# Kernel optimization log

Hardware: AMD Instinct MI355X
Metric: run time of the kernel (lower is better)

The kernel has to match this reference:

```python
import jax, jax.numpy as jnp
import numpy as np

DIM = 1280
HEADS = 16
HEAD_DIM = DIM // HEADS  # 80
N_CHUNKS = 8
CHUNK = 1024
TOTAL = N_CHUNKS * CHUNK  # 8192 packed tokens


def rotate_half(x):
    x1, x2 = jnp.split(x, 2, axis=-1)
    return jnp.concatenate([-x2, x1], axis=-1)


def setup_inputs() -> dict:
    key = jax.random.key(0)
    k0, k1, k2 = jax.random.split(key, 3)
    hidden_states = jax.random.normal(k0, (TOTAL, DIM), dtype=jnp.float32)
    # 2D-rope style per-token angles, duplicated halves (standard vision RoPE layout)
    inv_freq = 1.0 / (10000.0 ** (jnp.arange(0, HEAD_DIM, 2, dtype=jnp.float32) / HEAD_DIM))
    pos = jnp.arange(TOTAL, dtype=jnp.float32)
    freqs = pos[:, None] * inv_freq[None, :]            # [T, HEAD_DIM//2]
    emb = jnp.concatenate([freqs, freqs], axis=-1)      # [T, HEAD_DIM]
    cos = jnp.cos(emb)
    sin = jnp.sin(emb)
    qkv_w = jax.random.normal(k1, (3 * DIM, DIM), dtype=jnp.float32) * 0.02
    qkv_b = jnp.zeros((3 * DIM,), dtype=jnp.float32)
    proj_w = jax.random.normal(k2, (DIM, DIM), dtype=jnp.float32) * 0.02
    proj_b = jnp.zeros((DIM,), dtype=jnp.float32)
    cu_seqlens = (jnp.arange(N_CHUNKS + 1, dtype=jnp.int32) * CHUNK)
    return {"hidden_states": hidden_states, "cos": cos, "sin": sin,
            "qkv_w": qkv_w, "qkv_b": qkv_b, "proj_w": proj_w, "proj_b": proj_b,
            "cu_seqlens": cu_seqlens}


def reference(hidden_states, cos, sin, qkv_w, qkv_b, proj_w, proj_b, cu_seqlens):
    # Equal-length chunks (cu_seqlens uniform): vectorize the Python chunk loop
    # as a leading batch axis n over chunks of length L.
    n = cu_seqlens.shape[0] - 1
    total, dim = hidden_states.shape
    L = total // n
    scaling = HEAD_DIM ** -0.5

    x = hidden_states.reshape(n, L, dim)
    qkv = x @ qkv_w.T + qkv_b                              # [n, L, 3*dim]
    qkv = qkv.reshape(n, L, 3, HEADS, HEAD_DIM)
    q, k, v = qkv[:, :, 0], qkv[:, :, 1], qkv[:, :, 2]     # [n, L, H, hd]

    # inline RoPE in fp32 (matches apply_rotary_pos_emb_vision)
    c = cos.reshape(n, L, 1, HEAD_DIM).astype(jnp.float32)
    s = sin.reshape(n, L, 1, HEAD_DIM).astype(jnp.float32)
    qf = q.astype(jnp.float32)
    kf = k.astype(jnp.float32)
    q = (qf * c + rotate_half(qf) * s).astype(q.dtype)
    k = (kf * c + rotate_half(kf) * s).astype(k.dtype)

    # naive per-chunk full attention: QK^T, fp32 softmax, PV
    scores = jnp.einsum('nlhd,nmhd->nhlm', q, k) * scaling  # [n, H, L, L]
    probs = jax.nn.softmax(scores.astype(jnp.float32), axis=-1).astype(q.dtype)
    out = jnp.einsum('nhlm,nmhd->nlhd', probs, v)           # [n, L, H, hd]
    out = out.reshape(n, L, dim)
    out = out @ proj_w.T + proj_b                           # [n, L, dim]
    return out.reshape(total, dim)
```

## Files before the change

### kernel.cpp

```cpp
#include <hip/hip_runtime.h>
#include <stdint.h>

#define DIM 1280
#define HEADS 16
#define HD 80
#define TOTAL 8192
#define CHUNK 1024
#define QKVN 3840

typedef __attribute__((ext_vector_type(8))) __bf16 bf16x8;
typedef __attribute__((ext_vector_type(4))) float floatx4;

typedef __attribute__((address_space(1))) const uint32_t gu32;
typedef __attribute__((address_space(3))) uint32_t lu32;

__device__ __forceinline__ void llds16(const void* g, void* l) {
  __builtin_amdgcn_global_load_lds((gu32*)g, (lu32*)l, 16, 0, 0);
}

__device__ __forceinline__ unsigned short f2b(float f) {
  union { __bf16 b; unsigned short u; } x; x.b = (__bf16)f; return x.u;
}
__device__ __forceinline__ float b2f(unsigned short u) {
  union { __bf16 b; unsigned short u; } x; x.u = u; return (float)x.b;
}
__device__ __forceinline__ float fexp2(float x) {
#if __has_builtin(__builtin_amdgcn_exp2f)
  return __builtin_amdgcn_exp2f(x);
#else
  return __expf(x * 0.6931471805599453f);
#endif
}

#define QSCALE (0.11180339887498949f * 1.44269504088896340f)

#define QROW 96
#define KT_SH (64 * 104)
#define VT_SH (80 * 72)

__global__ void cvt_bf16(const float* __restrict__ src, unsigned short* __restrict__ dst, int n4) {
  int i = blockIdx.x * 256 + threadIdx.x;
  if (i >= n4) return;
  float4 v = reinterpret_cast<const float4*>(src)[i];
  ushort4 o;
  o.x = f2b(v.x); o.y = f2b(v.y); o.z = f2b(v.z); o.w = f2b(v.w);
  reinterpret_cast<ushort4*>(dst)[i] = o;
}

template<int MODE>
__launch_bounds__(256, 2)
__global__ void gemm_bt(const unsigned short* __restrict__ A,
                        const unsigned short* __restrict__ B,
                        const float* __restrict__ bias,
                        unsigned short* __restrict__ qo,
                        unsigned short* __restrict__ ko,
                        unsigned short* __restrict__ vo,
                        float* __restrict__ fo) {
  __shared__ __attribute__((aligned(16))) unsigned short lsA[128 * 32];
  __shared__ __attribute__((aligned(16))) unsigned short lsB[128 * 32];
  const int m0 = blockIdx.x * 128;
  const int n0 = blockIdx.y * 128;
  const int tid = threadIdx.x;
  const int wv = tid >> 6, lane = tid & 63;
  const int wr = wv >> 1, wc = wv & 1;
  const int q4 = lane >> 4, l15 = lane & 15;

  floatx4 acc[4][4];
#pragma unroll
  for (int i = 0; i < 4; ++i)
#pragma unroll
    for (int j = 0; j < 4; ++j)
      acc[i][j] = (floatx4){0.f, 0.f, 0.f, 0.f};

  const int srow = lane >> 2;
  const int sslot = lane & 3;

  for (int kk = 0; kk < DIM; kk += 32) {
    __syncthreads();
#pragma unroll
    for (int t = 0; t < 2; ++t) {
      const int rbase = wv * 32 + t * 16;
      const int r = rbase + srow;
      const int sg = sslot ^ ((r >> 1) & 3);
      llds16(A + (size_t)(m0 + r) * DIM + kk + sg * 8, &lsA[rbase * 32]);
      llds16(B + (size_t)(n0 + r) * DIM + kk + sg * 8, &lsB[rbase * 32]);
    }
    __syncthreads();
    bf16x8 af[4], bfr[4];
#pragma unroll
    for (int i = 0; i < 4; ++i) {
      const int r = wr * 64 + i * 16 + l15;
      af[i] = *reinterpret_cast<const bf16x8*>(&lsA[r * 32 + ((q4 ^ ((r >> 1) & 3)) << 3)]);
      const int c = wc * 64 + i * 16 + l15;
      bfr[i] = *reinterpret_cast<const bf16x8*>(&lsB[c * 32 + ((q4 ^ ((c >> 1) & 3)) << 3)]);
    }
#pragma unroll
    for (int i = 0; i < 4; ++i)
#pragma unroll
      for (int j = 0; j < 4; ++j)
        acc[i][j] = __builtin_amdgcn_mfma_f32_16x16x32_bf16(af[i], bfr[j], acc[i][j], 0, 0, 0);
  }

#pragma unroll
  for (int i = 0; i < 4; ++i) {
#pragma unroll
    for (int j = 0; j < 4; ++j) {
      const int n = n0 + wc * 64 + j * 16 + l15;
      const float bn = bias[n];
#pragma unroll
      for (int r = 0; r < 4; ++r) {
        const int m = m0 + wr * 64 + i * 16 + q4 * 4 + r;
        const float val = acc[i][j][r] + bn;
        if (MODE == 0) {
          if (n < DIM)            qo[(size_t)m * DIM + n] = f2b(val);
          else if (n < 2 * DIM)   ko[(size_t)m * DIM + (n - DIM)] = f2b(val);
          else                    vo[(size_t)m * DIM + (n - 2 * DIM)] = f2b(val);
        } else {
          fo[(size_t)m * DIM + n] = val;
        }
      }
    }
  }
}

__global__ void prep_q(const unsigned short* __restrict__ qbuf,
                       const float* __restrict__ cp, const float* __restrict__ sp,
                       unsigned short* __restrict__ qimg) {
  const int m = blockIdx.x, tid = threadIdx.x;
  const int ch = m >> 10, rl = m & 1023;
#pragma unroll
  for (int i = 0; i < 3; ++i) {
    const int it = i * 256 + tid;
    if (it < 640) {
      const int h = it / 40, d = it - h * 40;
      const float c = cp[m * HD + d], s = sp[m * HD + d];
      const float x1 = b2f(qbuf[(size_t)m * DIM + h * HD + d]);
      const float x2 = b2f(qbuf[(size_t)m * DIM + h * HD + d + 40]);
      const size_t ob = ((size_t)(ch * 16 + h) * 1024 + rl) * QROW;
      qimg[ob + d]      = f2b((x1 * c - x2 * s) * QSCALE);
      qimg[ob + d + 40] = f2b((x2 * c + x1 * s) * QSCALE);
    }
  }
  { const int h = tid >> 4, c = tid & 15;
    qimg[((size_t)(ch * 16 + h) * 1024 + rl) * QROW + 80 + c] = 0; }
}

__global__ void prep_k(const unsigned short* __restrict__ kbuf,
                       const float* __restrict__ cp, const float* __restrict__ sp,
                       unsigned short* __restrict__ kimg) {
  const int m = blockIdx.x, tid = threadIdx.x;
  const int ch = m >> 10, rl = m & 1023;
  const int jt = rl >> 6, rr = rl & 63;
#pragma unroll
  for (int i = 0; i < 3; ++i) {
    const int it = i * 256 + tid;
    if (it < 640) {
      const int h = it / 40, d = it - h * 40;
      const float c = cp[m * HD + d], s = sp[m * HD + d];
      const float x1 = b2f(kbuf[(size_t)m * DIM + h * HD + d]);
      const float x2 = b2f(kbuf[(size_t)m * DIM + h * HD + d + 40]);
      const size_t ob = ((size_t)((ch * 16 + h) * 16 + jt) * KT_SH) + rr * 104;
      kimg[ob + d]      = f2b(x1 * c - x2 * s);
      kimg[ob + d + 40] = f2b(x2 * c + x1 * s);
    }
  }
#pragma unroll
  for (int i = 0; i < 2; ++i) {
    const int it = i * 256 + tid;
    if (it < 384) {
      const int h = it / 24, c = it - h * 24;
      kimg[((size_t)((ch * 16 + h) * 16 + jt) * KT_SH) + rr * 104 + 80 + c] = 0;
    }
  }
}

__global__ void prep_v(const unsigned short* __restrict__ vbuf,
                       unsigned short* __restrict__ vimg) {
  __shared__ __attribute__((aligned(16))) unsigned short lsT[64 * 88];
  const int bx = blockIdx.x;
  const int jt = bx & 15, h = (bx >> 4) & 15, ch = bx >> 8;
  const int tid = threadIdx.x;
  const int row0 = ch * CHUNK + jt * 64;
#pragma unroll
  for (int i = 0; i < 3; ++i) {
    const int it = i * 256 + tid;
    if (it < 640) {
      const int r = it / 10, c = it - r * 10;
      const uint4 v = *reinterpret_cast<const uint4*>(vbuf + (size_t)(row0 + r) * DIM + h * HD + c * 8);
      *reinterpret_cast<uint4*>(&lsT[r * 88 + c * 8]) = v;
    }
  }
  __syncthreads();
  unsigned short* ot = vimg + (size_t)((ch * 16 + h) * 16 + jt) * VT_SH;
#pragma unroll
  for (int i = 0; i < 12; ++i) {
    const int it = i * 256 + tid;
    if (it < 2880) {
      const int d = it / 36, kk = it - d * 36;
      uint32_t w = 0;
      if (kk < 32) {
        const uint32_t lo = lsT[(2 * kk) * 88 + d];
        const uint32_t hi = lsT[(2 * kk + 1) * 88 + d];
        w = lo | (hi << 16);
      }
      *reinterpret_cast<uint32_t*>(ot + d * 72 + kk * 2) = w;
    }
  }
}

__launch_bounds__(256, 3)
__global__ void attn_k(const unsigned short* __restrict__ qimg,
                       const unsigned short* __restrict__ kimg,
                       const unsigned short* __restrict__ vimg,
                       unsigned short* __restrict__ ob) {
  __shared__ __attribute__((aligned(16))) unsigned short lsK[KT_SH];
  __shared__ __attribute__((aligned(16))) unsigned short lsV[VT_SH];
  __shared__ __attribute__((aligned(16))) unsigned short lsP[128 * 72];

  const int bx = blockIdx.x;
  const int qt = bx & 7, h = (bx >> 3) & 15, ch = bx >> 7;
  const int tid = threadIdx.x, wv = tid >> 6, lane = tid & 63;
  const int q4 = lane >> 4, l15 = lane & 15;
  const int qrow_loc = qt * 128 + wv * 32;

  bf16x8 aq[2][3];
  {
    const unsigned short* qb = qimg + ((size_t)(ch * 16 + h) * 1024 + qrow_loc) * QROW;
#pragma unroll
    for (int mt = 0; mt < 2; ++mt)
#pragma unroll
      for (int ks = 0; ks < 3; ++ks)
        aq[mt][ks] = *reinterpret_cast<const bf16x8*>(qb + (size_t)(mt * 16 + l15) * QROW + ks * 32 + q4 * 8);
  }

  floatx4 oacc[2][5];
  float lpart[2] = {0.f, 0.f};
#pragma unroll
  for (int mt = 0; mt < 2; ++mt)
#pragma unroll
    for (int t = 0; t < 5; ++t) oacc[mt][t] = (floatx4){0.f, 0.f, 0.f, 0.f};

  const char* kbase = (const char*)(kimg + (size_t)(ch * 16 + h) * 16 * KT_SH);
  const char* vbase = (const char*)(vimg + (size_t)(ch * 16 + h) * 16 * VT_SH);

  for (int jt = 0; jt < 16; ++jt) {
    __syncthreads();
    {
      const char* kg = kbase + (size_t)jt * (KT_SH * 2);
#pragma unroll
      for (int r = 0; r < 4; ++r) {
        const int off = (r * 4 + wv) * 1024;
        if (off < KT_SH * 2)
          llds16(kg + off + lane * 16, (char*)lsK + off);
      }
      const char* vg = vbase + (size_t)jt * (VT_SH * 2);
#pragma unroll
      for (int r = 0; r < 3; ++r) {
        const int off = (r * 4 + wv) * 1024;
        if (off < VT_SH * 2) {
          if (off + 1024 <= VT_SH * 2) llds16(vg + off + lane * 16, (char*)lsV + off);
          else if (lane < 16)          llds16(vg + off + lane * 16, (char*)lsV + off);
        }
      }
    }
    __syncthreads();

    floatx4 sfr[2][4];
#pragma unroll
    for (int c = 0; c < 4; ++c) {
      const bf16x8 ak0 = *reinterpret_cast<const bf16x8*>(&lsK[(c * 16 + l15) * 104 + 0  + q4 * 8]);
      const bf16x8 ak1 = *reinterpret_cast<const bf16x8*>(&lsK[(c * 16 + l15) * 104 + 32 + q4 * 8]);
      const bf16x8 ak2 = *reinterpret_cast<const bf16x8*>(&lsK[(c * 16 + l15) * 104 + 64 + q4 * 8]);
#pragma unroll
      for (int mt = 0; mt < 2; ++mt) {
        floatx4 s = (floatx4){0.f, 0.f, 0.f, 0.f};
        s = __builtin_amdgcn_mfma_f32_16x16x32_bf16(ak0, aq[mt][0], s, 0, 0, 0);
        s = __builtin_amdgcn_mfma_f32_16x16x32_bf16(ak1, aq[mt][1], s, 0, 0, 0);
        s = __builtin_amdgcn_mfma_f32_16x16x32_bf16(ak2, aq[mt][2], s, 0, 0, 0);
        sfr[mt][c] = s;
      }
    }

#pragma unroll
    for (int mt = 0; mt < 2; ++mt)
#pragma unroll
      for (int c = 0; c < 4; ++c) {
        const float p0 = fexp2(sfr[mt][c][0]);
        const float p1 = fexp2(sfr[mt][c][1]);
        const float p2 = fexp2(sfr[mt][c][2]);
        const float p3 = fexp2(sfr[mt][c][3]);
        lpart[mt] += (p0 + p1) + (p2 + p3);
        ushort4 w;
        w.x = f2b(p0); w.y = f2b(p1); w.z = f2b(p2); w.w = f2b(p3);
        *reinterpret_cast<ushort4*>(&lsP[(wv * 32 + mt * 16 + l15) * 72 + c * 16 + q4 * 4]) = w;
      }

#pragma unroll
    for (int ks = 0; ks < 2; ++ks) {
      const bf16x8 ap0 = *reinterpret_cast<const bf16x8*>(&lsP[(wv * 32 + 0  + l15) * 72 + ks * 32 + q4 * 8]);
      const bf16x8 ap1 = *reinterpret_cast<const bf16x8*>(&lsP[(wv * 32 + 16 + l15) * 72 + ks * 32 + q4 * 8]);
#pragma unroll
      for (int t = 0; t < 5; ++t) {
        const bf16x8 bv = *reinterpret_cast<const bf16x8*>(&lsV[(t * 16 + l15) * 72 + ks * 32 + q4 * 8]);
        oacc[0][t] = __builtin_amdgcn_mfma_f32_16x16x32_bf16(ap0, bv, oacc[0][t], 0, 0, 0);
        oacc[1][t] = __builtin_amdgcn_mfma_f32_16x16x32_bf16(ap1, bv, oacc[1][t], 0, 0, 0);
      }
    }
  }

#pragma unroll
  for (int mt = 0; mt < 2; ++mt) {
    lpart[mt] += __shfl_xor(lpart[mt], 16, 64);
    lpart[mt] += __shfl_xor(lpart[mt], 32, 64);
  }
  float inv[2];
  inv[0] = 1.0f / lpart[0];
  inv[1] = 1.0f / lpart[1];

  float invr[2][4];
#pragma unroll
  for (int mt = 0; mt < 2; ++mt)
#pragma unroll
    for (int r = 0; r < 4; ++r)
      invr[mt][r] = __shfl(inv[mt], q4 * 4 + r, 64);

#pragma unroll
  for (int mt = 0; mt < 2; ++mt)
#pragma unroll
    for (int t = 0; t < 5; ++t)
#pragma unroll
      for (int r = 0; r < 4; ++r) {
        const int gr = ch * CHUNK + qrow_loc + mt * 16 + q4 * 4 + r;
        const int gc = h * HD + t * 16 + l15;
        ob[(size_t)gr * DIM + gc] = f2b(oacc[mt][t][r] * invr[mt][r]);
      }
}

extern "C" void kernel_launch(void* const* d_in, const int* in_sizes, int n_in,
                              void* d_out, int out_size, void* d_ws, size_t ws_size,
                              hipStream_t stream) {
  (void)in_sizes; (void)n_in; (void)out_size; (void)ws_size;
  const float* hs    = (const float*)d_in[0];
  const float* cosp  = (const float*)d_in[1];
  const float* sinp  = (const float*)d_in[2];
  const float* qkvw  = (const float*)d_in[3];
  const float* qkvb  = (const float*)d_in[4];
  const float* projw = (const float*)d_in[5];
  const float* projb = (const float*)d_in[6];

  char* ws = (char*)d_ws;
  unsigned short* xb   = (unsigned short*)(ws + 0);
  unsigned short* wq   = (unsigned short*)(ws + 20971520);
  unsigned short* qbuf = (unsigned short*)(ws + 30801920);
  unsigned short* kbuf = (unsigned short*)(ws + 51773440);
  unsigned short* vbuf = (unsigned short*)(ws + 72744960);
  unsigned short* wp   = (unsigned short*)(ws + 93716480);
  unsigned short* obuf = (unsigned short*)(ws + 96993280);
  unsigned short* kimg = (unsigned short*)(ws + 117964800);
  unsigned short* qimg = (unsigned short*)(ws + 0);
  unsigned short* vimg = (unsigned short*)(ws + 30801920);

  cvt_bf16<<<TOTAL * DIM / 4 / 256, 256, 0, stream>>>(hs, xb, TOTAL * DIM / 4);
  cvt_bf16<<<QKVN * DIM / 4 / 256, 256, 0, stream>>>(qkvw, wq, QKVN * DIM / 4);
  cvt_bf16<<<DIM * DIM / 4 / 256, 256, 0, stream>>>(projw, wp, DIM * DIM / 4);

  gemm_bt<0><<<dim3(TOTAL / 128, QKVN / 128), 256, 0, stream>>>(
      xb, wq, qkvb, qbuf, kbuf, vbuf, nullptr);

  prep_q<<<TOTAL, 256, 0, stream>>>(qbuf, cosp, sinp, qimg);
  prep_k<<<TOTAL, 256, 0, stream>>>(kbuf, cosp, sinp, kimg);
  prep_v<<<2048, 256, 0, stream>>>(vbuf, vimg);

  attn_k<<<1024, 256, 0, stream>>>(qimg, kimg, vimg, obuf);

  gemm_bt<1><<<dim3(TOTAL / 128, DIM / 128), 256, 0, stream>>>(
      obuf, wp, projb, nullptr, nullptr, nullptr, (float*)d_out);
}
```

Measured before the change: 383.4 us.

## Replace GEMM with 256x256 tile, 8-wave, double-buffered ping-pong pipeline

Rewrites both projection GEMMs to use 256x256 output tiles with 512 threads, a K-step of 64 and double-buffered LDS. Global-to-LDS loads for the next K-tile are split into four phases interleaved with MFMA blocks, using manual vmcnt waits, barriers and s_setprio. This aims to hide memory latency and raise arithmetic intensity over the single-buffered 128x128 kernel. The trade-offs are 128KB of LDS per block, which limits occupancy, and fewer blocks for the output projection GEMM (32x5 = 160 tiles), which may underfill the CUs.

```diff
diff --git a/kernel.cpp b/kernel.cpp
--- a/kernel.cpp
+++ b/kernel.cpp
@@ -47,77 +47,193 @@
   reinterpret_cast<ushort4*>(dst)[i] = o;
 }
 
+
+__device__ __forceinline__ void stage_a64(const unsigned short* __restrict__ G,
+                                          unsigned short* ls, int wv, int lane,
+                                          int row0, int kk, int hi) {
+#pragma unroll
+  for (int t = 0; t < 2; ++t) {
+    const int stripe = t * 8 + wv;
+    const int rb = ((stripe >> 3) << 7) + ((stripe & 7) << 3) + hi;
+    const int r = rb + (lane >> 3);
+    const int ch = (lane & 7) ^ (r & 7);
+    llds16(G + (size_t)(row0 + r) * DIM + kk + (ch << 3), ls + rb * 64);
+  }
+}
+
+__device__ __forceinline__ void stage_b64(const unsigned short* __restrict__ G,
+                                          unsigned short* ls, int wv, int lane,
+                                          int row0, int kk, int hi) {
+#pragma unroll
+  for (int t = 0; t < 2; ++t) {
+    const int stripe = t * 8 + wv;
+    const int rb = ((stripe >> 2) << 6) + ((stripe & 3) << 3) + hi;
+    const int r = rb + (lane >> 3);
+    const int ch = (lane & 7) ^ (r & 7);
+    llds16(G + (size_t)(row0 + r) * DIM + kk + (ch << 3), ls + rb * 64);
+  }
+}
+
+__device__ __forceinline__ bf16x8 frg(const unsigned short* ls, int r, int cx) {
+  return *reinterpret_cast<const bf16x8*>(ls + r * 64 + (cx << 3));
+}
+
+#define PH_PRE()                                          \
+  __builtin_amdgcn_s_barrier();                           \
+  asm volatile("s_waitcnt lgkmcnt(0)" ::: "memory");      \
+  __builtin_amdgcn_sched_barrier(0);                      \
+  __builtin_amdgcn_s_setprio(1)
+
+#define PH_POST() __builtin_amdgcn_s_setprio(0)
+
 template<int MODE>
-__launch_bounds__(256, 2)
-__global__ void gemm_bt(const unsigned short* __restrict__ A,
-                        const unsigned short* __restrict__ B,
-                        const float* __restrict__ bias,
-                        unsigned short* __restrict__ qo,
-                        unsigned short* __restrict__ ko,
-                        unsigned short* __restrict__ vo,
-                        float* __restrict__ fo) {
-  __shared__ __attribute__((aligned(16))) unsigned short lsA[128 * 32];
-  __shared__ __attribute__((aligned(16))) unsigned short lsB[128 * 32];
-  const int m0 = blockIdx.x * 128;
-  const int n0 = blockIdx.y * 128;
+__launch_bounds__(512, 2)
+__global__ void gemm8(const unsigned short* __restrict__ A,
+                      const unsigned short* __restrict__ B,
+                      const float* __restrict__ bias,
+                      unsigned short* __restrict__ qo,
+                      unsigned short* __restrict__ ko,
+                      unsigned short* __restrict__ vo,
+                      float* __restrict__ fo) {
+  __shared__ __attribute__((aligned(16))) unsigned short lsA[2][256 * 64];
+  __shared__ __attribute__((aligned(16))) unsigned short lsB[2][256 * 64];
+  const int m0 = blockIdx.x * 256;
+  const int n0 = blockIdx.y * 256;
   const int tid = threadIdx.x;
   const int wv = tid >> 6, lane = tid & 63;
-  const int wr = wv >> 1, wc = wv & 1;
+  const int wr = wv >> 2, wc = wv & 3;
   const int q4 = lane >> 4, l15 = lane & 15;
-
-  floatx4 acc[4][4];
-#pragma unroll
-  for (int i = 0; i < 4; ++i)
+  const int sx = l15 & 7;
+  const int cx0 = q4 ^ sx;
+  const int cx1 = (4 + q4) ^ sx;
+
+  stage_a64(A, &lsA[0][0], wv, lane, m0, 0, 0);
+  stage_b64(B, &lsB[0][0], wv, lane, n0, 0, 0);
+  stage_b64(B, &lsB[0][0], wv, lane, n0, 0, 32);
+  stage_a64(A, &lsA[0][0], wv, lane, m0, 0, 64);
+
+  floatx4 acc[8][4];
+#pragma unroll
+  for (int i = 0; i < 8; ++i)
 #pragma unroll
     for (int j = 0; j < 4; ++j)
       acc[i][j] = (floatx4){0.f, 0.f, 0.f, 0.f};
 
-  const int srow = lane >> 2;
-  const int sslot = lane & 3;
-
-  for (int kk = 0; kk < DIM; kk += 32) {
-    __syncthreads();
-#pragma unroll
-    for (int t = 0; t < 2; ++t) {
-      const int rbase = wv * 32 + t * 16;
-      const int r = rbase + srow;
-      const int sg = sslot ^ ((r >> 1) & 3);
-      llds16(A + (size_t)(m0 + r) * DIM + kk + sg * 8, &lsA[rbase * 32]);
-      llds16(B + (size_t)(n0 + r) * DIM + kk + sg * 8, &lsB[rbase * 32]);
-    }
-    __syncthreads();
-    bf16x8 af[4], bfr[4];
-#pragma unroll
-    for (int i = 0; i < 4; ++i) {
-      const int r = wr * 64 + i * 16 + l15;
-      af[i] = *reinterpret_cast<const bf16x8*>(&lsA[r * 32 + ((q4 ^ ((r >> 1) & 3)) << 3)]);
-      const int c = wc * 64 + i * 16 + l15;
-      bfr[i] = *reinterpret_cast<const bf16x8*>(&lsB[c * 32 + ((q4 ^ ((c >> 1) & 3)) << 3)]);
-    }
-#pragma unroll
-    for (int i = 0; i < 4; ++i)
-#pragma unroll
-      for (int j = 0; j < 4; ++j)
-        acc[i][j] = __builtin_amdgcn_mfma_f32_16x16x32_bf16(af[i], bfr[j], acc[i][j], 0, 0, 0);
-  }
-
-#pragma unroll
-  for (int i = 0; i < 4; ++i) {
-#pragma unroll
-    for (int j = 0; j < 4; ++j) {
-      const int n = n0 + wc * 64 + j * 16 + l15;
-      const float bn = bias[n];
+  asm volatile("s_waitcnt vmcnt(4)" ::: "memory");
+  __builtin_amdgcn_s_barrier();
+
+  const int rA = wr * 128 + l15;
+  const int rB = wc * 64 + l15;
+
+#pragma unroll 2
+  for (int kt = 0; kt < 20; ++kt) {
+    const unsigned short* la = &lsA[kt & 1][0];
+    const unsigned short* lb = &lsB[kt & 1][0];
+    unsigned short* sa = &lsA[(kt & 1) ^ 1][0];
+    unsigned short* sb = &lsB[(kt & 1) ^ 1][0];
+    const int kn = (kt + 1) * 64;
+    const bool st = (kt < 19);
+
+    bf16x8 Ar[4][2], Br[2][2];
+
+#pragma unroll
+    for (int m = 0; m < 4; ++m) {
+      Ar[m][0] = frg(la, rA + m * 16, cx0);
+      Ar[m][1] = frg(la, rA + m * 16, cx1);
+    }
+#pragma unroll
+    for (int n = 0; n < 2; ++n) {
+      Br[n][0] = frg(lb, rB + n * 16, cx0);
+      Br[n][1] = frg(lb, rB + n * 16, cx1);
+    }
+    if (st) stage_a64(A, sa, wv, lane, m0, kn, 0);
+    PH_PRE();
+#pragma unroll
+    for (int m = 0; m < 4; ++m)
+#pragma unroll
+      for (int n = 0; n < 2; ++n) {
+        acc[m][n] = __builtin_amdgcn_mfma_f32_16x16x32_bf16(Ar[m][0], Br[n][0], acc[m][n], 0, 0, 0);
+        acc[m][n] = __builtin_amdgcn_mfma_f32_16x16x32_bf16(Ar[m][1], Br[n][1], acc[m][n], 0, 0, 0);
+      }
+    PH_POST();
+    if (st) asm volatile("s_waitcnt vmcnt(4)" ::: "memory");
+    else    asm volatile("s_waitcnt vmcnt(2)" ::: "memory");
+    __builtin_amdgcn_s_barrier();
+
+#pragma unroll
+    for (int n = 0; n < 2; ++n) {
+      Br[n][0] = frg(lb, rB + (n + 2) * 16, cx0);
+      Br[n][1] = frg(lb, rB + (n + 2) * 16, cx1);
+    }
+    if (st) stage_b64(B, sb, wv, lane, n0, kn, 0);
+    PH_PRE();
+#pragma unroll
+    for (int m = 0; m < 4; ++m)
+#pragma unroll
+      for (int n = 0; n < 2; ++n) {
+        acc[m][n + 2] = __builtin_amdgcn_mfma_f32_16x16x32_bf16(Ar[m][0], Br[n][0], acc[m][n + 2], 0, 0, 0);
+        acc[m][n + 2] = __builtin_amdgcn_mfma_f32_16x16x32_bf16(Ar[m][1], Br[n][1], acc[m][n + 2], 0, 0, 0);
+      }
+    PH_POST();
+    if (st) asm volatile("s_waitcnt vmcnt(4)" ::: "memory");
+    else    asm volatile("s_waitcnt vmcnt(0)" ::: "memory");
+    __builtin_amdgcn_s_barrier();
+
+#pragma unroll
+    for (int m = 0; m < 4; ++m) {
+      Ar[m][0] = frg(la, rA + (m + 4) * 16, cx0);
+      Ar[m][1] = frg(la, rA + (m + 4) * 16, cx1);
+    }
+    if (st) stage_b64(B, sb, wv, lane, n0, kn, 32);
+    PH_PRE();
+#pragma unroll
+    for (int m = 0; m < 4; ++m)
+#pragma unroll
+      for (int n = 0; n < 2; ++n) {
+        acc[m + 4][n + 2] = __builtin_amdgcn_mfma_f32_16x16x32_bf16(Ar[m][0], Br[n][0], acc[m + 4][n + 2], 0, 0, 0);
+        acc[m + 4][n + 2] = __builtin_amdgcn_mfma_f32_16x16x32_bf16(Ar[m][1], Br[n][1], acc[m + 4][n + 2], 0, 0, 0);
+      }
+    PH_POST();
+    __builtin_amdgcn_s_barrier();
+
+#pragma unroll
+    for (int n = 0; n < 2; ++n) {
+      Br[n][0] = frg(lb, rB + n * 16, cx0);
+      Br[n][1] = frg(lb, rB + n * 16, cx1);
+    }
+    if (st) stage_a64(A, sa, wv, lane, m0, kn, 64);
+    PH_PRE();
+#pragma unroll
+    for (int m = 0; m < 4; ++m)
+#pragma unroll
+      for (int n = 0; n < 2; ++n) {
+        acc[m + 4][n] = __builtin_amdgcn_mfma_f32_16x16x32_bf16(Ar[m][0], Br[n][0], acc[m + 4][n], 0, 0, 0);
+        acc[m + 4][n] = __builtin_amdgcn_mfma_f32_16x16x32_bf16(Ar[m][1], Br[n][1], acc[m + 4][n], 0, 0, 0);
+      }
+    PH_POST();
+    if (st) asm volatile("s_waitcnt vmcnt(4)" ::: "memory");
+    __builtin_amdgcn_s_barrier();
+  }
+
+  unsigned short* os = nullptr;
+  int nloc = n0;
+  if (MODE == 0) {
+    if (blockIdx.y < 5)       { os = qo; }
+    else if (blockIdx.y < 10) { os = ko; nloc = n0 - DIM; }
+    else                      { os = vo; nloc = n0 - 2 * DIM; }
+  }
+#pragma unroll
+  for (int n = 0; n < 4; ++n) {
+    const int cg = wc * 64 + n * 16 + l15;
+    const float bn = bias[n0 + cg];
+#pragma unroll
+    for (int m = 0; m < 8; ++m) {
 #pragma unroll
       for (int r = 0; r < 4; ++r) {
-        const int m = m0 + wr * 64 + i * 16 + q4 * 4 + r;
-        const float val = acc[i][j][r] + bn;
-        if (MODE == 0) {
-          if (n < DIM)            qo[(size_t)m * DIM + n] = f2b(val);
-          else if (n < 2 * DIM)   ko[(size_t)m * DIM + (n - DIM)] = f2b(val);
-          else                    vo[(size_t)m * DIM + (n - 2 * DIM)] = f2b(val);
-        } else {
-          fo[(size_t)m * DIM + n] = val;
-        }
+        const int row = m0 + wr * 128 + m * 16 + q4 * 4 + r;
+        const float val = acc[m][n][r] + bn;
+        if (MODE == 0) os[(size_t)row * DIM + nloc + cg] = f2b(val);
+        else           fo[(size_t)row * DIM + n0 + cg] = val;
       }
     }
   }
@@ -364,7 +480,7 @@
   cvt_bf16<<<QKVN * DIM / 4 / 256, 256, 0, stream>>>(qkvw, wq, QKVN * DIM / 4);
   cvt_bf16<<<DIM * DIM / 4 / 256, 256, 0, stream>>>(projw, wp, DIM * DIM / 4);
 
-  gemm_bt<0><<<dim3(TOTAL / 128, QKVN / 128), 256, 0, stream>>>(
+  gemm8<0><<<dim3(TOTAL / 256, QKVN / 256), 512, 0, stream>>>(
       xb, wq, qkvb, qbuf, kbuf, vbuf, nullptr);
 
   prep_q<<<TOTAL, 256, 0, stream>>>(qbuf, cosp, sinp, qimg);
@@ -373,6 +489,6 @@
 
   attn_k<<<1024, 256, 0, stream>>>(qimg, kimg, vimg, obuf);
 
-  gemm_bt<1><<<dim3(TOTAL / 128, DIM / 128), 256, 0, stream>>>(
+  gemm8<1><<<dim3(TOTAL / 256, DIM / 256), 512, 0, stream>>>(
       obuf, wp, projb, nullptr, nullptr, nullptr, (float*)d_out);
 }
```

After: 380.3 us. Within noise of the previous version (-0.8%).
